# Kernel tuning notes

Hardware: AMD Instinct MI355X
Metric: run time of the kernel (lower is better)

Reference implementation:

```python
import jax, jax.numpy as jnp
import numpy as np

EPS = 1e-5

def _layernorm(h, g, b):
    m = jnp.mean(h, axis=-1, keepdims=True)
    v = jnp.mean((h - m) ** 2, axis=-1, keepdims=True)
    return (h - m) * jax.lax.rsqrt(v + EPS) * g + b

def setup_inputs() -> dict:
    B, N, D, H, C = 16, 4096, 1024, 512, 2
    key = jax.random.key(0)
    ks = jax.random.split(key, 16)
    def lin(k, fan_in, shape):
        return jax.random.normal(k, shape, dtype=jnp.float32) / np.sqrt(fan_in)
    return {
        "x":   jax.random.normal(ks[0], (B, N, D), dtype=jnp.float32),
        "W1":  lin(ks[1], D, (D, H)),  "b1": jnp.zeros((H,), jnp.float32),
        "g1":  jnp.ones((H,), jnp.float32), "beta1": jnp.zeros((H,), jnp.float32),
        "W2":  lin(ks[2], H, (H, H)),  "b2": jnp.zeros((H,), jnp.float32),
        "g2":  jnp.ones((H,), jnp.float32), "beta2": jnp.zeros((H,), jnp.float32),
        "Wa1": lin(ks[3], H, (H, H)),  "ba1": jnp.zeros((H,), jnp.float32),
        "wa2": lin(ks[4], H, (H, 1)),  "ba2": jnp.zeros((1,), jnp.float32),
        "Wc1": lin(ks[5], H, (H, H)),  "bc1": jnp.zeros((H,), jnp.float32),
        "Wc2": lin(ks[6], H, (H, C)),  "bc2": jnp.zeros((C,), jnp.float32),
    }

def reference(x, W1, b1, g1, beta1, W2, b2, g2, beta2,
              Wa1, ba1, wa2, ba2, Wc1, bc1, Wc2, bc2):
    # Feature extractor: Linear -> LayerNorm -> ReLU (x2); dropout is identity (eval)
    h = jax.nn.relu(_layernorm(jnp.einsum('bnd,dh->bnh', x, W1) + b1, g1, beta1))
    h = jax.nn.relu(_layernorm(jnp.einsum('bnh,hk->bnk', h, W2) + b2, g2, beta2))
    # Attention: Linear -> Tanh -> Linear(->1), softmax over instances (per bag)
    scores = jnp.tanh(jnp.einsum('bnh,hk->bnk', h, Wa1) + ba1) @ wa2 + ba2  # [B,N,1]
    attn = jax.nn.softmax(scores, axis=1)                                   # [B,N,1]
    pooled = jnp.sum(h * attn, axis=1)                                      # [B,H]
    # Classifier (no sample_source path): Linear -> ReLU -> Linear
    logits = jax.nn.relu(pooled @ Wc1 + bc1) @ Wc2 + bc2                    # [B,C]
    return logits
```

## Files before the change

### kernel.cpp

```cpp
#include <hip/hip_runtime.h>
#include <hip/hip_bf16.h>


#define MTOT   65536
#define DDIM   1024
#define HDIM   512
#define NBAG   16
#define NINST  4096

typedef __attribute__((ext_vector_type(8))) short bf16x8;
typedef __attribute__((ext_vector_type(4))) float f32x4;

__device__ __forceinline__ unsigned short f2bf(float f) {
  __hip_bfloat16 h = __float2bfloat16(f);
  unsigned short u;
  __builtin_memcpy(&u, &h, 2);
  return u;
}
__device__ __forceinline__ float bf2f(unsigned short u) {
  unsigned int x = ((unsigned int)u) << 16;
  float f;
  __builtin_memcpy(&f, &x, 4);
  return f;
}

__device__ __forceinline__ void gload16(const void* g, void* l) {
  __builtin_amdgcn_global_load_lds(
      (const __attribute__((address_space(1))) unsigned int*)g,
      (__attribute__((address_space(3))) unsigned int*)l, 16, 0, 0);
}

__device__ __forceinline__ bf16x8 pack8(float4 a, float4 b) {
  bf16x8 r;
  r[0] = (short)f2bf(a.x); r[1] = (short)f2bf(a.y);
  r[2] = (short)f2bf(a.z); r[3] = (short)f2bf(a.w);
  r[4] = (short)f2bf(b.x); r[5] = (short)f2bf(b.y);
  r[6] = (short)f2bf(b.z); r[7] = (short)f2bf(b.w);
  return r;
}

__global__ void transpose_cast(const float* __restrict__ src,
                               __hip_bfloat16* __restrict__ dst,
                               int R, int C) {
  __shared__ float t[32][33];
  const int c0 = blockIdx.x * 32, r0 = blockIdx.y * 32;
  const int tx = threadIdx.x, ty = threadIdx.y;
#pragma unroll
  for (int i = 0; i < 32; i += 8)
    t[ty + i][tx] = src[(size_t)(r0 + ty + i) * C + c0 + tx];
  __syncthreads();
#pragma unroll
  for (int i = 0; i < 32; i += 8)
    dst[(size_t)(c0 + ty + i) * R + r0 + tx] = __float2bfloat16(t[tx][ty + i]);
}

#define BM 128
#define BN 128
#define BK 64

template <int KD, bool AF32, int MODE>
__global__ __launch_bounds__(256, AF32 ? 2 : 3)
void gemm_tile(const void* Ap, const __hip_bfloat16* __restrict__ BT,
               const float* __restrict__ bias,
               __hip_bfloat16* __restrict__ ybuf,
               float2* __restrict__ statp,
               const float* __restrict__ wa2,
               float* __restrict__ scorep) {
  __shared__ __align__(16) char smem[32768];
  __hip_bfloat16* AtP = (__hip_bfloat16*)smem;
  __hip_bfloat16* BtP = (__hip_bfloat16*)(smem + 16384);

  const int tid  = threadIdx.x;
  const int lane = tid & 63;
  const int w    = tid >> 6;
  const int wm   = w >> 1;
  const int wn   = w & 1;
  const int l16  = lane & 15;
  const int lg   = lane >> 4;

  const int cpx = gridDim.x >> 3;
  int bid = blockIdx.x;
  bid = (bid & 7) * cpx + (bid >> 3);
  const int n_blk   = bid & 3;
  const int row_blk = bid >> 2;
  const size_t row0 = (size_t)row_blk * BM;
  const int col0    = n_blk * BN;

  const int rS   = lane & 15;
  const int sS   = (lane >> 4) ^ (lane & 3);
  const int dOff = lane * 8;
  const int frag_off = l16 * 8 + ((lg ^ (l16 & 3)) << 7);

  constexpr int NT = KD / BK;
  const __hip_bfloat16* Abf = (const __hip_bfloat16*)Ap;
  const float* Af32 = (const float*)Ap;

  f32x4 acc[4][4];
#pragma unroll
  for (int i = 0; i < 4; i++)
#pragma unroll
    for (int j = 0; j < 4; j++) acc[i][j] = (f32x4){0.f, 0.f, 0.f, 0.f};

  auto stageB = [&](int kb) {
#pragma unroll
    for (int i = 0; i < 4; i++) {
      const int c = w * 4 + i;
      const int rg = (c >> 1) * 16 + rS;
      const int kc = kb + (c & 1) * 32 + sS * 8;
      gload16(BT + (size_t)(col0 + rg) * KD + kc, BtP + c * 512 + dOff);
    }
  };
  auto stageA_g = [&](int kb) {
#pragma unroll
    for (int i = 0; i < 4; i++) {
      const int c = w * 4 + i;
      const int rg = (c >> 1) * 16 + rS;
      const int kc = kb + (c & 1) * 32 + sS * 8;
      gload16(Abf + (row0 + rg) * KD + kc, AtP + c * 512 + dOff);
    }
  };

  float4 ra[2][8];
#define LOADA_(S, KB)                                                          \
  _Pragma("unroll") for (int i = 0; i < 4; i++) {                              \
    const int c_ = w * 4 + i;                                                  \
    const float* gp_ = Af32 + (row0 + (c_ >> 1) * 16 + rS) * KD + (KB) +       \
                       (c_ & 1) * 32 + sS * 8;                                 \
    ra[S][i * 2 + 0] = *(const float4*)gp_;                                    \
    ra[S][i * 2 + 1] = *(const float4*)(gp_ + 4);                              \
  }
#define WRITEA_(S)                                                             \
  _Pragma("unroll") for (int i = 0; i < 4; i++) {                              \
    *reinterpret_cast<bf16x8*>(AtP + (w * 4 + i) * 512 + dOff) =               \
        pack8(ra[S][i * 2 + 0], ra[S][i * 2 + 1]);                             \
  }

#define COMPUTE_STEP                                                           \
  _Pragma("unroll") for (int h = 0; h < 2; h++) {                              \
    bf16x8 af[4], bfr[4];                                                      \
    _Pragma("unroll") for (int fm = 0; fm < 4; fm++)                           \
        af[fm] = *reinterpret_cast<const bf16x8*>(                             \
            AtP + ((wm * 4 + fm) * 2 + h) * 512 + frag_off);                   \
    _Pragma("unroll") for (int fn = 0; fn < 4; fn++)                           \
        bfr[fn] = *reinterpret_cast<const bf16x8*>(                            \
            BtP + ((wn * 4 + fn) * 2 + h) * 512 + frag_off);                   \
    _Pragma("unroll") for (int fm = 0; fm < 4; fm++)                           \
    _Pragma("unroll") for (int fn = 0; fn < 4; fn++)                           \
        acc[fm][fn] = __builtin_amdgcn_mfma_f32_16x16x32_bf16(                 \
            af[fm], bfr[fn], acc[fm][fn], 0, 0, 0);                            \
  }

  if constexpr (AF32) {
    LOADA_(0, 0);
    for (int tb = 0; tb < NT; tb += 2) {
      {
        WRITEA_(0);
        stageB(tb * BK);
        __syncthreads();
        if (tb + 1 < NT) { LOADA_(1, (tb + 1) * BK); }
        COMPUTE_STEP
        __syncthreads();
      }
      {
        WRITEA_(1);
        stageB((tb + 1) * BK);
        __syncthreads();
        if (tb + 2 < NT) { LOADA_(0, (tb + 2) * BK); }
        COMPUTE_STEP
        __syncthreads();
      }
    }
  } else {
    for (int t = 0; t < NT; ++t) {
      stageA_g(t * BK);
      stageB(t * BK);
      __syncthreads();
      COMPUTE_STEP
      __syncthreads();
    }
  }
#undef LOADA_
#undef WRITEA_
#undef COMPUTE_STEP

  float* redS = (float*)smem;
  float* redQ = (float*)smem + 256;

  float biasv[4];
#pragma unroll
  for (int fn = 0; fn < 4; fn++)
    biasv[fn] = bias[col0 + wn * 64 + fn * 16 + l16];

  if (MODE == 0) {
#pragma unroll
    for (int fm = 0; fm < 4; fm++)
#pragma unroll
      for (int r = 0; r < 4; r++) {
        const int rl = wm * 64 + fm * 16 + lg * 4 + r;
        float s1 = 0.f, s2 = 0.f;
#pragma unroll
        for (int fn = 0; fn < 4; fn++) {
          const float z = acc[fm][fn][r] + biasv[fn];
          s1 += z;
          s2 += z * z;
          ybuf[(row0 + rl) * HDIM + col0 + wn * 64 + fn * 16 + l16] =
              __float2bfloat16(z);
        }
#pragma unroll
        for (int m = 1; m < 16; m <<= 1) {
          s1 += __shfl_xor(s1, m);
          s2 += __shfl_xor(s2, m);
        }
        if (l16 == 0) {
          redS[rl * 2 + wn] = s1;
          redQ[rl * 2 + wn] = s2;
        }
      }
    __syncthreads();
    if (tid < BM) {
      statp[(row0 + tid) * 4 + n_blk] =
          make_float2(redS[tid * 2] + redS[tid * 2 + 1],
                      redQ[tid * 2] + redQ[tid * 2 + 1]);
    }
  } else {
    float wv[4];
#pragma unroll
    for (int fn = 0; fn < 4; fn++)
      wv[fn] = wa2[col0 + wn * 64 + fn * 16 + l16];
#pragma unroll
    for (int fm = 0; fm < 4; fm++)
#pragma unroll
      for (int r = 0; r < 4; r++) {
        const int rl = wm * 64 + fm * 16 + lg * 4 + r;
        float s = 0.f;
#pragma unroll
        for (int fn = 0; fn < 4; fn++) {
          const float z = acc[fm][fn][r] + biasv[fn];
          s += tanhf(z) * wv[fn];
        }
#pragma unroll
        for (int m = 1; m < 16; m <<= 1) s += __shfl_xor(s, m);
        if (l16 == 0) redS[rl * 2 + wn] = s;
      }
    __syncthreads();
    if (tid < BM) {
      scorep[(row0 + tid) * 4 + n_blk] = redS[tid * 2] + redS[tid * 2 + 1];
    }
  }
}

__global__ __launch_bounds__(256)
void ln_apply(__hip_bfloat16* __restrict__ y,
              const float2* __restrict__ statp,
              const float* __restrict__ g, const float* __restrict__ be) {
  const int row = blockIdx.x * 4 + (threadIdx.x >> 6);
  const int c0 = (threadIdx.x & 63) * 8;
  const float2* sp = statp + (size_t)row * 4;
  float S = 0.f, Q = 0.f;
#pragma unroll
  for (int j = 0; j < 4; j++) {
    const float2 p = sp[j];
    S += p.x;
    Q += p.y;
  }
  const float mu = S * (1.f / 512.f);
  const float var = Q * (1.f / 512.f) - mu * mu;
  const float rs = rsqrtf(var + 1e-5f);

  __hip_bfloat16* yp = y + (size_t)row * HDIM + c0;
  bf16x8 v = *reinterpret_cast<const bf16x8*>(yp);
  const float4 ga = *(const float4*)(g + c0), gb = *(const float4*)(g + c0 + 4);
  const float4 ba = *(const float4*)(be + c0), bb = *(const float4*)(be + c0 + 4);
  float gv[8] = {ga.x, ga.y, ga.z, ga.w, gb.x, gb.y, gb.z, gb.w};
  float bv[8] = {ba.x, ba.y, ba.z, ba.w, bb.x, bb.y, bb.z, bb.w};
  bf16x8 o;
#pragma unroll
  for (int j = 0; j < 8; j++) {
    const float f = bf2f((unsigned short)v[j]);
    const float h = fmaxf((f - mu) * rs * gv[j] + bv[j], 0.f);
    o[j] = (short)f2bf(h);
  }
  *reinterpret_cast<bf16x8*>(yp) = o;
}

__global__ void softmax_bag(const float* __restrict__ scorep,
                            const float* __restrict__ ba2,
                            float* __restrict__ at) {
  const int b = blockIdx.x;
  const int tid = threadIdx.x;
  const int lane = tid & 63, w = tid >> 6;
  const float bv = ba2[0];
  float v[16];
  float mx = -1e30f;
#pragma unroll
  for (int i = 0; i < 16; i++) {
    const float4 sp = *reinterpret_cast<const float4*>(
        scorep + ((size_t)b * NINST + tid + i * 256) * 4);
    v[i] = sp.x + sp.y + sp.z + sp.w + bv;
    mx = fmaxf(mx, v[i]);
  }
#pragma unroll
  for (int off = 32; off; off >>= 1) mx = fmaxf(mx, __shfl_xor(mx, off));
  __shared__ float red[4];
  if (lane == 0) red[w] = mx;
  __syncthreads();
  mx = fmaxf(fmaxf(red[0], red[1]), fmaxf(red[2], red[3]));
  float sum = 0.f;
#pragma unroll
  for (int i = 0; i < 16; i++) {
    v[i] = expf(v[i] - mx);
    sum += v[i];
  }
#pragma unroll
  for (int off = 32; off; off >>= 1) sum += __shfl_xor(sum, off);
  __shared__ float red2[4];
  if (lane == 0) red2[w] = sum;
  __syncthreads();
  sum = red2[0] + red2[1] + red2[2] + red2[3];
  const float inv = 1.f / sum;
#pragma unroll
  for (int i = 0; i < 16; i++) at[(size_t)b * NINST + tid + i * 256] = v[i] * inv;
}

__global__ void pooled_partial(const __hip_bfloat16* __restrict__ h2,
                               const float* __restrict__ at,
                               float* __restrict__ part) {
  const int bid = blockIdx.x;
  const int b = bid >> 5, cc = (bid >> 3) & 3, nch = bid & 7;
  const int tid = threadIdx.x;
  const int c4 = (tid & 31) * 4, sub = tid >> 5;
  const int n0 = nch * 512;
  const size_t base = (size_t)b * NINST;
  float a0 = 0.f, a1 = 0.f, a2 = 0.f, a3 = 0.f;
  for (int n = n0 + sub; n < n0 + 512; n += 8) {
    const float a = at[base + n];
    const ushort4 u = *reinterpret_cast<const ushort4*>(
        &h2[(base + n) * HDIM + cc * 128 + c4]);
    a0 += a * bf2f(u.x);
    a1 += a * bf2f(u.y);
    a2 += a * bf2f(u.z);
    a3 += a * bf2f(u.w);
  }
  __shared__ float pb[8][128];
  pb[sub][c4 + 0] = a0;
  pb[sub][c4 + 1] = a1;
  pb[sub][c4 + 2] = a2;
  pb[sub][c4 + 3] = a3;
  __syncthreads();
  if (tid < 128) {
    float s = 0.f;
#pragma unroll
    for (int j = 0; j < 8; j++) s += pb[j][tid];
    part[(size_t)nch * 8192 + b * 512 + cc * 128 + tid] = s;
  }
}

__global__ void pooled_reduce(const float* __restrict__ part,
                              float* __restrict__ pooled) {
  const int i = blockIdx.x * 256 + threadIdx.x;
  float s = 0.f;
#pragma unroll
  for (int j = 0; j < 8; j++) s += part[(size_t)j * 8192 + i];
  pooled[i] = s;
}

__global__ void classifier(const float* __restrict__ pooled,
                           const float* __restrict__ Wc1,
                           const float* __restrict__ bc1,
                           const float* __restrict__ Wc2,
                           const float* __restrict__ bc2,
                           float* __restrict__ out) {
  __shared__ float P[NBAG][512];
  __shared__ float Rb[NBAG][512];
  const int tid = threadIdx.x;
#pragma unroll
  for (int i = 0; i < NBAG; i++) P[i][tid] = pooled[i * 512 + tid];
  __syncthreads();
  float r[NBAG];
#pragma unroll
  for (int i = 0; i < NBAG; i++) r[i] = 0.f;
  for (int k = 0; k < 512; k++) {
    const float wv = Wc1[k * 512 + tid];
#pragma unroll
    for (int i = 0; i < NBAG; i++) r[i] += P[i][k] * wv;
  }
#pragma unroll
  for (int i = 0; i < NBAG; i++) Rb[i][tid] = fmaxf(r[i] + bc1[tid], 0.f);
  __syncthreads();
  if (tid < 32) {
    const int i = tid >> 1, c = tid & 1;
    float s = bc2[c];
    for (int k = 0; k < 512; k++) s += Rb[i][k] * Wc2[k * 2 + c];
    out[i * 2 + c] = s;
  }
}

extern "C" void kernel_launch(void* const* d_in, const int* in_sizes, int n_in,
                              void* d_out, int out_size, void* d_ws,
                              size_t ws_size, hipStream_t stream) {
  const float* x   = (const float*)d_in[0];
  const float* W1  = (const float*)d_in[1];
  const float* b1  = (const float*)d_in[2];
  const float* g1  = (const float*)d_in[3];
  const float* be1 = (const float*)d_in[4];
  const float* W2  = (const float*)d_in[5];
  const float* b2  = (const float*)d_in[6];
  const float* g2  = (const float*)d_in[7];
  const float* be2 = (const float*)d_in[8];
  const float* Wa1 = (const float*)d_in[9];
  const float* ba1 = (const float*)d_in[10];
  const float* wa2 = (const float*)d_in[11];
  const float* ba2 = (const float*)d_in[12];
  const float* Wc1 = (const float*)d_in[13];
  const float* bc1 = (const float*)d_in[14];
  const float* Wc2 = (const float*)d_in[15];
  const float* bc2 = (const float*)d_in[16];
  float* out = (float*)d_out;

  char* ws = (char*)d_ws;
  __hip_bfloat16* W1T = (__hip_bfloat16*)(ws + 0);
  __hip_bfloat16* W2T = (__hip_bfloat16*)(ws + 1048576);
  __hip_bfloat16* WaT = (__hip_bfloat16*)(ws + 1572864);
  float2* statp  = (float2*)(ws + 2097152);
  float* scorep  = (float*)(ws + 4194304);
  float* attn    = (float*)(ws + 5242880);
  float* part    = (float*)(ws + 5505024);
  float* pooled  = (float*)(ws + 5767168);
  __hip_bfloat16* buf1 = (__hip_bfloat16*)(ws + 8388608);
  __hip_bfloat16* buf2 = (__hip_bfloat16*)(ws + 75497472);

  transpose_cast<<<dim3(16, 32), dim3(32, 8), 0, stream>>>(W1, W1T, DDIM, HDIM);
  transpose_cast<<<dim3(16, 16), dim3(32, 8), 0, stream>>>(W2, W2T, HDIM, HDIM);
  transpose_cast<<<dim3(16, 16), dim3(32, 8), 0, stream>>>(Wa1, WaT, HDIM, HDIM);

  const int grid = (MTOT / BM) * (HDIM / BN);

  gemm_tile<DDIM, true, 0><<<grid, 256, 0, stream>>>(
      x, W1T, b1, buf1, statp, nullptr, nullptr);
  ln_apply<<<MTOT / 4, 256, 0, stream>>>(buf1, statp, g1, be1);

  gemm_tile<HDIM, false, 0><<<grid, 256, 0, stream>>>(
      buf1, W2T, b2, buf2, statp, nullptr, nullptr);
  ln_apply<<<MTOT / 4, 256, 0, stream>>>(buf2, statp, g2, be2);

  gemm_tile<HDIM, false, 1><<<grid, 256, 0, stream>>>(
      buf2, WaT, ba1, nullptr, nullptr, wa2, scorep);

  softmax_bag<<<NBAG, 256, 0, stream>>>(scorep, ba2, attn);
  pooled_partial<<<512, 256, 0, stream>>>(buf2, attn, part);
  pooled_reduce<<<32, 256, 0, stream>>>(part, pooled);
  classifier<<<1, 512, 0, stream>>>(pooled, Wc1, bc1, Wc2, bc2, out);
}
```

Before: 447.3 us.

## Use 256x256 double-buffered GEMM tiles with interleaved prefetch and MFMA scheduling

The GEMM kernel moves from 128x128 tiles with 4 waves to 256x256 tiles with 8 waves. LDS is double-buffered (128KB) and global loads for the next k-step are interleaved with four MFMA phases, using explicit waitcnt, sched barriers and setprio. The larger tile raises arithmetic intensity and the schedule is meant to hide load latency. The LN-stat and score partial layouts drop from 4 to 2 column blocks. The trade-off is higher register and LDS pressure, fewer blocks in the grid, and a more fragile hand-written schedule.

```diff
diff --git a/kernel.cpp b/kernel.cpp
--- a/kernel.cpp
+++ b/kernel.cpp
@@ -39,6 +39,11 @@
   return r;
 }
 
+#define VMW(N) asm volatile("s_waitcnt vmcnt(" #N ")" ::: "memory")
+#define LKW0   asm volatile("s_waitcnt lgkmcnt(0)" ::: "memory")
+#define SB0    __builtin_amdgcn_sched_barrier(0)
+#define BARRIER __builtin_amdgcn_s_barrier()
+
 __global__ void transpose_cast(const float* __restrict__ src,
                                __hip_bfloat16* __restrict__ dst,
                                int R, int C) {
@@ -54,156 +59,210 @@
     dst[(size_t)(c0 + ty + i) * R + r0 + tx] = __float2bfloat16(t[tx][ty + i]);
 }
 
-#define BM 128
-#define BN 128
+#define BM 256
+#define BN 256
 #define BK 64
 
 template <int KD, bool AF32, int MODE>
-__global__ __launch_bounds__(256, AF32 ? 2 : 3)
+__global__ __launch_bounds__(512, 2)
 void gemm_tile(const void* Ap, const __hip_bfloat16* __restrict__ BT,
                const float* __restrict__ bias,
                __hip_bfloat16* __restrict__ ybuf,
                float2* __restrict__ statp,
                const float* __restrict__ wa2,
                float* __restrict__ scorep) {
-  __shared__ __align__(16) char smem[32768];
-  __hip_bfloat16* AtP = (__hip_bfloat16*)smem;
-  __hip_bfloat16* BtP = (__hip_bfloat16*)(smem + 16384);
+  __shared__ __align__(16) char smem[131072];
 
   const int tid  = threadIdx.x;
   const int lane = tid & 63;
   const int w    = tid >> 6;
-  const int wm   = w >> 1;
-  const int wn   = w & 1;
+  const int wm   = w >> 2;
+  const int wn   = w & 3;
   const int l16  = lane & 15;
   const int lg   = lane >> 4;
+
+  const int rS = lane & 15;
+  const int sS = (lane >> 4) ^ (lane & 3);
+  const int frag_off = l16 * 8 + ((lg ^ (l16 & 3)) << 7);
 
   const int cpx = gridDim.x >> 3;
   int bid = blockIdx.x;
   bid = (bid & 7) * cpx + (bid >> 3);
-  const int n_blk   = bid & 3;
-  const int row_blk = bid >> 2;
-  const size_t row0 = (size_t)row_blk * BM;
-  const int col0    = n_blk * BN;
-
-  const int rS   = lane & 15;
-  const int sS   = (lane >> 4) ^ (lane & 3);
-  const int dOff = lane * 8;
-  const int frag_off = l16 * 8 + ((lg ^ (l16 & 3)) << 7);
+  const int n_blk = bid & 1;
+  const size_t row0 = (size_t)(bid >> 1) * BM;
+  const int col0 = n_blk * BN;
 
   constexpr int NT = KD / BK;
   const __hip_bfloat16* Abf = (const __hip_bfloat16*)Ap;
   const float* Af32 = (const float*)Ap;
 
-  f32x4 acc[4][4];
-#pragma unroll
-  for (int i = 0; i < 4; i++)
+  f32x4 acc[8][4];
+#pragma unroll
+  for (int i = 0; i < 8; i++)
 #pragma unroll
     for (int j = 0; j < 4; j++) acc[i][j] = (f32x4){0.f, 0.f, 0.f, 0.f};
 
-  auto stageB = [&](int kb) {
-#pragma unroll
-    for (int i = 0; i < 4; i++) {
-      const int c = w * 4 + i;
-      const int rg = (c >> 1) * 16 + rS;
-      const int kc = kb + (c & 1) * 32 + sS * 8;
-      gload16(BT + (size_t)(col0 + rg) * KD + kc, BtP + c * 512 + dOff);
-    }
-  };
-  auto stageA_g = [&](int kb) {
-#pragma unroll
-    for (int i = 0; i < 4; i++) {
-      const int c = w * 4 + i;
-      const int rg = (c >> 1) * 16 + rS;
-      const int kc = kb + (c & 1) * 32 + sS * 8;
-      gload16(Abf + (row0 + rg) * KD + kc, AtP + c * 512 + dOff);
-    }
-  };
-
-  float4 ra[2][8];
-#define LOADA_(S, KB)                                                          \
-  _Pragma("unroll") for (int i = 0; i < 4; i++) {                              \
-    const int c_ = w * 4 + i;                                                  \
-    const float* gp_ = Af32 + (row0 + (c_ >> 1) * 16 + rS) * KD + (KB) +       \
-                       (c_ & 1) * 32 + sS * 8;                                 \
-    ra[S][i * 2 + 0] = *(const float4*)gp_;                                    \
-    ra[S][i * 2 + 1] = *(const float4*)(gp_ + 4);                              \
-  }
-#define WRITEA_(S)                                                             \
-  _Pragma("unroll") for (int i = 0; i < 4; i++) {                              \
-    *reinterpret_cast<bf16x8*>(AtP + (w * 4 + i) * 512 + dOff) =               \
-        pack8(ra[S][i * 2 + 0], ra[S][i * 2 + 1]);                             \
-  }
-
-#define COMPUTE_STEP                                                           \
-  _Pragma("unroll") for (int h = 0; h < 2; h++) {                              \
-    bf16x8 af[4], bfr[4];                                                      \
-    _Pragma("unroll") for (int fm = 0; fm < 4; fm++)                           \
-        af[fm] = *reinterpret_cast<const bf16x8*>(                             \
-            AtP + ((wm * 4 + fm) * 2 + h) * 512 + frag_off);                   \
-    _Pragma("unroll") for (int fn = 0; fn < 4; fn++)                           \
-        bfr[fn] = *reinterpret_cast<const bf16x8*>(                            \
-            BtP + ((wn * 4 + fn) * 2 + h) * 512 + frag_off);                   \
-    _Pragma("unroll") for (int fm = 0; fm < 4; fm++)                           \
-    _Pragma("unroll") for (int fn = 0; fn < 4; fn++)                           \
-        acc[fm][fn] = __builtin_amdgcn_mfma_f32_16x16x32_bf16(                 \
-            af[fm], bfr[fn], acc[fm][fn], 0, 0, 0);                            \
-  }
+  auto ldsA = [&](int buf, int h) -> __hip_bfloat16* {
+    return (__hip_bfloat16*)(smem + buf * 32768 + h * 16384);
+  };
+  auto ldsB = [&](int buf, int h) -> __hip_bfloat16* {
+    return (__hip_bfloat16*)(smem + 65536 + buf * 32768 + h * 16384);
+  };
+
+  auto stageB_h = [&](int kb, int buf, int h) {
+#pragma unroll
+    for (int j = 0; j < 2; j++) {
+      const int c = w + j * 8;
+      gload16(BT + (size_t)(col0 + c * 16 + rS) * KD + kb + h * 32 + sS * 8,
+              ldsB(buf, h) + c * 512 + lane * 8);
+    }
+  };
+  auto stageA_h = [&](int kb, int buf, int h) {
+#pragma unroll
+    for (int j = 0; j < 2; j++) {
+      const int c = w + j * 8;
+      gload16(Abf + (row0 + c * 16 + rS) * KD + kb + h * 32 + sS * 8,
+              ldsA(buf, h) + c * 512 + lane * 8);
+    }
+  };
+
+  float4 set0[4], set1[4];
+  auto loadF32 = [&](float4* s, int kb, int h) {
+#pragma unroll
+    for (int j = 0; j < 2; j++) {
+      const float* gp =
+          Af32 + (row0 + (w + j * 8) * 16 + rS) * KD + kb + h * 32 + sS * 8;
+      s[j * 2 + 0] = *(const float4*)gp;
+      s[j * 2 + 1] = *(const float4*)(gp + 4);
+    }
+  };
+  auto cvtWrite = [&](const float4* s, int buf, int h) {
+#pragma unroll
+    for (int j = 0; j < 2; j++)
+      *reinterpret_cast<bf16x8*>(ldsA(buf, h) + (w + j * 8) * 512 + lane * 8) =
+          pack8(s[j * 2 + 0], s[j * 2 + 1]);
+  };
+
+  auto rdA = [&](bf16x8* af, int buf, int h, int mh) {
+#pragma unroll
+    for (int f = 0; f < 4; f++)
+      af[f] = *reinterpret_cast<const bf16x8*>(
+          ldsA(buf, h) + (wm * 8 + mh * 4 + f) * 512 + frag_off);
+  };
+  auto rdB = [&](bf16x8* bf, int buf, int h) {
+#pragma unroll
+    for (int n = 0; n < 4; n++)
+      bf[n] = *reinterpret_cast<const bf16x8*>(
+          ldsB(buf, h) + (wn * 4 + n) * 512 + frag_off);
+  };
+  auto mfma16 = [&](int m0, const bf16x8* af, const bf16x8* bf) {
+#pragma unroll
+    for (int f = 0; f < 4; f++)
+#pragma unroll
+      for (int n = 0; n < 4; n++)
+        acc[m0 + f][n] = __builtin_amdgcn_mfma_f32_16x16x32_bf16(
+            af[f], bf[n], acc[m0 + f][n], 0, 0, 0);
+  };
 
   if constexpr (AF32) {
-    LOADA_(0, 0);
-    for (int tb = 0; tb < NT; tb += 2) {
-      {
-        WRITEA_(0);
-        stageB(tb * BK);
-        __syncthreads();
-        if (tb + 1 < NT) { LOADA_(1, (tb + 1) * BK); }
-        COMPUTE_STEP
-        __syncthreads();
+    loadF32(set0, 0, 0);
+    stageB_h(0, 0, 0);
+    loadF32(set1, 0, 1);
+    stageB_h(0, 0, 1);
+    cvtWrite(set0, 0, 0);
+    VMW(6);
+    LKW0;
+    BARRIER;
+  } else {
+    stageA_h(0, 0, 0);
+    stageB_h(0, 0, 0);
+    stageA_h(0, 0, 1);
+    stageB_h(0, 0, 1);
+    VMW(4);
+    BARRIER;
+  }
+
+#pragma unroll 2
+  for (int t = 0; t < NT; ++t) {
+    const int cur = t & 1, nxt = cur ^ 1;
+    const bool pf = (t + 1 < NT);
+    const int kbn = (t + 1) * BK;
+    bf16x8 af[4], bf0[4], bf1[4];
+
+    rdA(af, cur, 0, 0);
+    rdB(bf0, cur, 0);
+    if constexpr (AF32) {
+      cvtWrite(set1, cur, 1);
+      if (pf) loadF32(set0, kbn, 0);
+    } else {
+      if (pf) stageA_h(kbn, nxt, 0);
+    }
+    BARRIER;
+    LKW0; SB0;
+    __builtin_amdgcn_s_setprio(1);
+    mfma16(0, af, bf0);
+    __builtin_amdgcn_s_setprio(0);
+    BARRIER;
+
+    rdA(af, cur, 0, 1);
+    if (pf) stageB_h(kbn, nxt, 0);
+    BARRIER;
+    LKW0; SB0;
+    __builtin_amdgcn_s_setprio(1);
+    mfma16(4, af, bf0);
+    __builtin_amdgcn_s_setprio(0);
+    if constexpr (AF32) { VMW(6); } else { VMW(4); }
+    BARRIER;
+
+    rdA(af, cur, 1, 0);
+    rdB(bf1, cur, 1);
+    if constexpr (AF32) {
+      if (pf) {
+        cvtWrite(set0, nxt, 0);
+        loadF32(set1, kbn, 1);
       }
-      {
-        WRITEA_(1);
-        stageB((tb + 1) * BK);
-        __syncthreads();
-        if (tb + 2 < NT) { LOADA_(0, (tb + 2) * BK); }
-        COMPUTE_STEP
-        __syncthreads();
-      }
-    }
-  } else {
-    for (int t = 0; t < NT; ++t) {
-      stageA_g(t * BK);
-      stageB(t * BK);
-      __syncthreads();
-      COMPUTE_STEP
-      __syncthreads();
-    }
-  }
-#undef LOADA_
-#undef WRITEA_
-#undef COMPUTE_STEP
-
+    } else {
+      if (pf) stageA_h(kbn, nxt, 1);
+    }
+    BARRIER;
+    LKW0; SB0;
+    __builtin_amdgcn_s_setprio(1);
+    mfma16(0, af, bf1);
+    __builtin_amdgcn_s_setprio(0);
+    BARRIER;
+
+    rdA(af, cur, 1, 1);
+    if (pf) stageB_h(kbn, nxt, 1);
+    BARRIER;
+    LKW0; SB0;
+    __builtin_amdgcn_s_setprio(1);
+    mfma16(4, af, bf1);
+    __builtin_amdgcn_s_setprio(0);
+    if constexpr (AF32) { VMW(6); } else { VMW(4); }
+    BARRIER;
+  }
+
+  __syncthreads();
   float* redS = (float*)smem;
-  float* redQ = (float*)smem + 256;
+  float* redQ = (float*)(smem + 4096);
 
   float biasv[4];
 #pragma unroll
-  for (int fn = 0; fn < 4; fn++)
-    biasv[fn] = bias[col0 + wn * 64 + fn * 16 + l16];
+  for (int n = 0; n < 4; n++) biasv[n] = bias[col0 + wn * 64 + n * 16 + l16];
 
   if (MODE == 0) {
 #pragma unroll
-    for (int fm = 0; fm < 4; fm++)
+    for (int f = 0; f < 8; f++)
 #pragma unroll
       for (int r = 0; r < 4; r++) {
-        const int rl = wm * 64 + fm * 16 + lg * 4 + r;
+        const int rl = wm * 128 + f * 16 + lg * 4 + r;
         float s1 = 0.f, s2 = 0.f;
 #pragma unroll
-        for (int fn = 0; fn < 4; fn++) {
-          const float z = acc[fm][fn][r] + biasv[fn];
+        for (int n = 0; n < 4; n++) {
+          const float z = acc[f][n][r] + biasv[n];
           s1 += z;
           s2 += z * z;
-          ybuf[(row0 + rl) * HDIM + col0 + wn * 64 + fn * 16 + l16] =
+          ybuf[(row0 + rl) * HDIM + col0 + wn * 64 + n * 16 + l16] =
               __float2bfloat16(z);
         }
 #pragma unroll
@@ -212,39 +271,41 @@
           s2 += __shfl_xor(s2, m);
         }
         if (l16 == 0) {
-          redS[rl * 2 + wn] = s1;
-          redQ[rl * 2 + wn] = s2;
+          redS[rl * 4 + wn] = s1;
+          redQ[rl * 4 + wn] = s2;
         }
       }
     __syncthreads();
     if (tid < BM) {
-      statp[(row0 + tid) * 4 + n_blk] =
-          make_float2(redS[tid * 2] + redS[tid * 2 + 1],
-                      redQ[tid * 2] + redQ[tid * 2 + 1]);
+      const float S = redS[tid * 4] + redS[tid * 4 + 1] + redS[tid * 4 + 2] +
+                      redS[tid * 4 + 3];
+      const float Q = redQ[tid * 4] + redQ[tid * 4 + 1] + redQ[tid * 4 + 2] +
+                      redQ[tid * 4 + 3];
+      statp[(row0 + tid) * 2 + n_blk] = make_float2(S, Q);
     }
   } else {
     float wv[4];
 #pragma unroll
-    for (int fn = 0; fn < 4; fn++)
-      wv[fn] = wa2[col0 + wn * 64 + fn * 16 + l16];
-#pragma unroll
-    for (int fm = 0; fm < 4; fm++)
+    for (int n = 0; n < 4; n++) wv[n] = wa2[col0 + wn * 64 + n * 16 + l16];
+#pragma unroll
+    for (int f = 0; f < 8; f++)
 #pragma unroll
       for (int r = 0; r < 4; r++) {
-        const int rl = wm * 64 + fm * 16 + lg * 4 + r;
+        const int rl = wm * 128 + f * 16 + lg * 4 + r;
         float s = 0.f;
 #pragma unroll
-        for (int fn = 0; fn < 4; fn++) {
-          const float z = acc[fm][fn][r] + biasv[fn];
-          s += tanhf(z) * wv[fn];
+        for (int n = 0; n < 4; n++) {
+          const float z = acc[f][n][r] + biasv[n];
+          s += tanhf(z) * wv[n];
         }
 #pragma unroll
         for (int m = 1; m < 16; m <<= 1) s += __shfl_xor(s, m);
-        if (l16 == 0) redS[rl * 2 + wn] = s;
+        if (l16 == 0) redS[rl * 4 + wn] = s;
       }
     __syncthreads();
     if (tid < BM) {
-      scorep[(row0 + tid) * 4 + n_blk] = redS[tid * 2] + redS[tid * 2 + 1];
+      scorep[(row0 + tid) * 2 + n_blk] = redS[tid * 4] + redS[tid * 4 + 1] +
+                                         redS[tid * 4 + 2] + redS[tid * 4 + 3];
     }
   }
 }
@@ -255,14 +316,9 @@
               const float* __restrict__ g, const float* __restrict__ be) {
   const int row = blockIdx.x * 4 + (threadIdx.x >> 6);
   const int c0 = (threadIdx.x & 63) * 8;
-  const float2* sp = statp + (size_t)row * 4;
-  float S = 0.f, Q = 0.f;
-#pragma unroll
-  for (int j = 0; j < 4; j++) {
-    const float2 p = sp[j];
-    S += p.x;
-    Q += p.y;
-  }
+  const float2 p0 = statp[(size_t)row * 2 + 0];
+  const float2 p1 = statp[(size_t)row * 2 + 1];
+  const float S = p0.x + p1.x, Q = p0.y + p1.y;
   const float mu = S * (1.f / 512.f);
   const float var = Q * (1.f / 512.f) - mu * mu;
   const float rs = rsqrtf(var + 1e-5f);
@@ -294,9 +350,9 @@
   float mx = -1e30f;
 #pragma unroll
   for (int i = 0; i < 16; i++) {
-    const float4 sp = *reinterpret_cast<const float4*>(
-        scorep + ((size_t)b * NINST + tid + i * 256) * 4);
-    v[i] = sp.x + sp.y + sp.z + sp.w + bv;
+    const float2 sp = *reinterpret_cast<const float2*>(
+        scorep + ((size_t)b * NINST + tid + i * 256) * 2);
+    v[i] = sp.x + sp.y + bv;
     mx = fmaxf(mx, v[i]);
   }
 #pragma unroll
@@ -435,15 +491,15 @@
 
   const int grid = (MTOT / BM) * (HDIM / BN);
 
-  gemm_tile<DDIM, true, 0><<<grid, 256, 0, stream>>>(
+  gemm_tile<DDIM, true, 0><<<grid, 512, 0, stream>>>(
       x, W1T, b1, buf1, statp, nullptr, nullptr);
   ln_apply<<<MTOT / 4, 256, 0, stream>>>(buf1, statp, g1, be1);
 
-  gemm_tile<HDIM, false, 0><<<grid, 256, 0, stream>>>(
+  gemm_tile<HDIM, false, 0><<<grid, 512, 0, stream>>>(
       buf1, W2T, b2, buf2, statp, nullptr, nullptr);
   ln_apply<<<MTOT / 4, 256, 0, stream>>>(buf2, statp, g2, be2);
 
-  gemm_tile<HDIM, false, 1><<<grid, 256, 0, stream>>>(
+  gemm_tile<HDIM, false, 1><<<grid, 512, 0, stream>>>(
       buf2, WaT, ba1, nullptr, nullptr, wa2, scorep);
 
   softmax_bag<<<NBAG, 256, 0, stream>>>(scorep, ba2, attn);
```

After: 440.9 us. No clear change (-1.4%).
